# Performance work log

Measured on AMD Instinct MI355X. Metric: run time of the kernel, lower is better.

## Reference

```python
import jax, jax.numpy as jnp
import numpy as np

B, S, E = 2, 2048, 2048
H, D = 16, 128  # num_attention_heads, head_dim = hidden_size // num_heads


def rotate_half(x):
    x1 = x[..., : x.shape[-1] // 2]
    x2 = x[..., x.shape[-1] // 2 :]
    return jnp.concatenate((-x2, x1), axis=-1)


def setup_inputs() -> dict:
    key = jax.random.key(0)
    ks = jax.random.split(key, 7)
    return {
        "hidden_states": jax.random.normal(ks[0], (B, S, E), dtype=jnp.float32),
        "cos": jax.random.uniform(ks[1], (1, 1, S, D), dtype=jnp.float32),
        "sin": jax.random.uniform(ks[2], (1, 1, S, D), dtype=jnp.float32),
        "wq": jax.random.normal(ks[3], (E, H * D), dtype=jnp.float32) / np.sqrt(E),
        "wk": jax.random.normal(ks[4], (E, H * D), dtype=jnp.float32) / np.sqrt(E),
        "wv": jax.random.normal(ks[5], (E, H * D), dtype=jnp.float32) / np.sqrt(E),
        "wo": jax.random.normal(ks[6], (H * D, E), dtype=jnp.float32) / np.sqrt(H * D),
    }


def reference(hidden_states, cos, sin, wq, wk, wv, wo):
    # QKV projections (no bias, per attention_bias=False)
    q = (hidden_states @ wq).reshape(B, S, H, D).transpose(0, 2, 1, 3)  # bhsd
    k = (hidden_states @ wk).reshape(B, S, H, D).transpose(0, 2, 1, 3)
    v = (hidden_states @ wv).reshape(B, S, H, D).transpose(0, 2, 1, 3)
    # RoPE (applied after the head transpose, as in the original)
    q = q * cos + rotate_half(q) * sin
    k = k * cos + rotate_half(k) * sin
    # NOTE: original forward never applies self.scaling and uses no causal mask.
    scores = jnp.einsum("bhqd,bhkd->bhqk", q, k)
    attn = jax.nn.softmax(scores.astype(jnp.float32), axis=-1)
    out = jnp.einsum("bhqk,bhkd->bhqd", attn, v)
    out = out.transpose(0, 2, 1, 3).reshape(B, S, H * D)
    return out @ wo
```

## Files before the change

### kernel.cpp

```cpp
#include <hip/hip_runtime.h>
#include <stdint.h>

typedef _Float16 f16;
typedef _Float16 half8 __attribute__((ext_vector_type(8)));
typedef _Float16 half4 __attribute__((ext_vector_type(4)));
typedef __fp16 fp16x2 __attribute__((ext_vector_type(2)));
typedef float f32x4 __attribute__((ext_vector_type(4)));
typedef float f32x16 __attribute__((ext_vector_type(16)));
typedef uint32_t u32x4 __attribute__((ext_vector_type(4)));

static constexpr int Bsz = 2, S = 2048, E = 2048, H = 16, D = 128;
static constexpr int M = Bsz * S;
static constexpr int N_QKV = 3 * H * D;
static constexpr int HD = H * D;

__device__ __forceinline__ void gload_lds16(const void* gp, void* lp) {
  __builtin_amdgcn_global_load_lds(
      (const __attribute__((address_space(1))) uint32_t*)(uintptr_t)gp,
      (__attribute__((address_space(3))) uint32_t*)(uint32_t)(uintptr_t)lp,
      16, 0, 0);
}

__device__ __forceinline__ uint32_t pkrtz(float a, float b) {
  fp16x2 r = __builtin_amdgcn_cvt_pkrtz(a, b);
  return __builtin_bit_cast(uint32_t, r);
}

__global__ void cast_f32_f16(const float* __restrict__ in, f16* __restrict__ out) {
  size_t i = (size_t)(blockIdx.x * 256 + threadIdx.x) * 8;
  float4 a = *(const float4*)&in[i];
  float4 b = *(const float4*)&in[i + 4];
  half8 h;
  h[0] = (f16)a.x; h[1] = (f16)a.y; h[2] = (f16)a.z; h[3] = (f16)a.w;
  h[4] = (f16)b.x; h[5] = (f16)b.y; h[6] = (f16)b.z; h[7] = (f16)b.w;
  *(half8*)&out[i] = h;
}

__global__ void transpose_cast(const float* __restrict__ wq, const float* __restrict__ wk,
                               const float* __restrict__ wv, const float* __restrict__ wo,
                               f16* __restrict__ wt, f16* __restrict__ wot) {
  __shared__ float tile[32][33];
  int z = blockIdx.z;
  const float* src = (z == 0) ? wq : (z == 1) ? wk : (z == 2) ? wv : wo;
  f16* dst = (z == 3) ? wot : wt + (size_t)z * E * HD;
  int bx = blockIdx.x * 32, by = blockIdx.y * 32;
  int tx = threadIdx.x, ty = threadIdx.y;
#pragma unroll
  for (int r = 0; r < 4; ++r)
    tile[ty + r * 8][tx] = src[(size_t)(by + ty + r * 8) * 2048 + bx + tx];
  __syncthreads();
#pragma unroll
  for (int r = 0; r < 4; ++r)
    dst[(size_t)(bx + ty + r * 8) * 2048 + by + tx] = (f16)tile[tx][ty + r * 8];
}

template <typename OutT>
__global__ __launch_bounds__(256, 4) void gemm_bt(const f16* __restrict__ A,
                                                  const f16* __restrict__ Bt,
                                                  OutT* __restrict__ C,
                                                  int Mm, int Nn, int Kk) {
  __shared__ f16 As[128 * 32];
  __shared__ f16 Bs[128 * 32];
  const int t = threadIdx.x, l = t & 63;
  const int wm = (t >> 7) & 1, wn = (t >> 6) & 1;
  const int bm = blockIdx.x, bn = blockIdx.y;
  const int lr = l & 15, g = l >> 4;
  const int srow = t >> 2;
  const int schunk = t & 3;
  const int scol = ((schunk ^ (srow & 3)) * 8);
  const size_t abase = (size_t)(bm * 128 + srow) * Kk;
  const size_t bbase = (size_t)(bn * 128 + srow) * Kk;
  f32x4 acc[4][4] = {};
  for (int k0 = 0; k0 < Kk; k0 += 32) {
    __syncthreads();
    gload_lds16(&A[abase + k0 + scol], &As[t * 8]);
    gload_lds16(&A[abase + (size_t)64 * Kk + k0 + scol], &As[2048 + t * 8]);
    gload_lds16(&Bt[bbase + k0 + scol], &Bs[t * 8]);
    gload_lds16(&Bt[bbase + (size_t)64 * Kk + k0 + scol], &Bs[2048 + t * 8]);
    __syncthreads();
    half8 af[4], bf[4];
#pragma unroll
    for (int i = 0; i < 4; ++i) {
      int ra = wm * 64 + i * 16 + lr;
      int rb = wn * 64 + i * 16 + lr;
      af[i] = *(const half8*)&As[ra * 32 + ((g ^ (ra & 3)) * 8)];
      bf[i] = *(const half8*)&Bs[rb * 32 + ((g ^ (rb & 3)) * 8)];
    }
#pragma unroll
    for (int i = 0; i < 4; ++i)
#pragma unroll
      for (int j = 0; j < 4; ++j)
        acc[i][j] = __builtin_amdgcn_mfma_f32_16x16x32_f16(af[i], bf[j], acc[i][j], 0, 0, 0);
  }
#pragma unroll
  for (int i = 0; i < 4; ++i)
#pragma unroll
    for (int j = 0; j < 4; ++j) {
      int row = bm * 128 + wm * 64 + i * 16 + g * 4;
      int col = bn * 128 + wn * 64 + j * 16 + lr;
#pragma unroll
      for (int r = 0; r < 4; ++r)
        C[(size_t)(row + r) * Nn + col] = (OutT)acc[i][j][r];
    }
}

__global__ void rope_split(const f16* __restrict__ qkv, const float* __restrict__ cosb,
                           const float* __restrict__ sinb, f16* __restrict__ Q,
                           f16* __restrict__ Ko) {
  int idx = blockIdx.x * 256 + threadIdx.x;
  int d4 = idx & 15;
  int h = (idx >> 4) & 15;
  int s = (idx >> 8) & 2047;
  int b = idx >> 19;
  int d = d4 * 4;
  size_t mrow = (size_t)(b * S + s) * N_QKV;
  const f16* q = &qkv[mrow + h * D];
  const f16* k = &qkv[mrow + HD + h * D];
  size_t ob = ((size_t)(b * H + h) * S + s) * D;
  float4 c1 = *(const float4*)&cosb[s * D + d];
  float4 c2 = *(const float4*)&cosb[s * D + 64 + d];
  float4 s1 = *(const float4*)&sinb[s * D + d];
  float4 s2 = *(const float4*)&sinb[s * D + 64 + d];
  float c1a[4] = {c1.x, c1.y, c1.z, c1.w}, c2a[4] = {c2.x, c2.y, c2.z, c2.w};
  float s1a[4] = {s1.x, s1.y, s1.z, s1.w}, s2a[4] = {s2.x, s2.y, s2.z, s2.w};
  half4 qlo = *(const half4*)&q[d], qhi = *(const half4*)&q[d + 64];
  half4 klo = *(const half4*)&k[d], khi = *(const half4*)&k[d + 64];
  half4 oql, oqh, okl, okh;
#pragma unroll
  for (int j = 0; j < 4; ++j) {
    float ql = (float)qlo[j], qh = (float)qhi[j];
    float kl = (float)klo[j], kh = (float)khi[j];
    oql[j] = (f16)(ql * c1a[j] - qh * s1a[j]);
    oqh[j] = (f16)(qh * c2a[j] + ql * s2a[j]);
    okl[j] = (f16)(kl * c1a[j] - kh * s1a[j]);
    okh[j] = (f16)(kh * c2a[j] + kl * s2a[j]);
  }
  *(half4*)&Q[ob + d] = oql;  *(half4*)&Q[ob + d + 64] = oqh;
  *(half4*)&Ko[ob + d] = okl; *(half4*)&Ko[ob + d + 64] = okh;
}

__global__ void transpose_v(const f16* __restrict__ qkv, f16* __restrict__ VtG) {
  __shared__ f16 tl[64][136];
  int bid = blockIdx.x;
  int bh = bid >> 5, st = bid & 31;
  int b = bh >> 4, h = bh & 15;
  int t = threadIdx.x;
  int s0 = st * 64;
#pragma unroll
  for (int rnd = 0; rnd < 4; ++rnd) {
    int row = rnd * 16 + (t >> 4);
    int ch = t & 15;
    half8 v = *(const half8*)&qkv[(size_t)(b * S + s0 + row) * N_QKV + 2 * HD + h * D + ch * 8];
    *(half8*)&tl[row][ch * 8] = v;
  }
  __syncthreads();
#pragma unroll
  for (int rnd = 0; rnd < 4; ++rnd) {
    int d = rnd * 32 + (t >> 3);
    int ch = t & 7;
    half8 v;
#pragma unroll
    for (int j = 0; j < 8; ++j) v[j] = tl[ch * 8 + j][d];
    *(half8*)&VtG[((size_t)bh * D + d) * S + s0 + ch * 8] = v;
  }
}

__device__ __forceinline__ void stage_kv(const f16* __restrict__ Kg, const f16* __restrict__ Vg,
                                         f16* KsB, f16* VsB, int t, int kv) {
#pragma unroll
  for (int rnd = 0; rnd < 4; ++rnd) {
    int row = rnd * 16 + (t >> 4);
    int c = t & 15;
    gload_lds16(&Kg[(size_t)(kv + row) * D + ((c ^ (row & 7)) * 8)], &KsB[rnd * 2048 + t * 8]);
  }
#pragma unroll
  for (int rnd = 0; rnd < 4; ++rnd) {
    int row = rnd * 32 + (t >> 3);
    int c = t & 7;
    gload_lds16(&Vg[(size_t)row * S + kv + ((c ^ (row & 7)) * 8)], &VsB[rnd * 2048 + t * 8]);
  }
}

__global__ __launch_bounds__(256, 2) void flash_attn2(const f16* __restrict__ Q,
                                                      const f16* __restrict__ K,
                                                      const f16* __restrict__ Vt,
                                                      f16* __restrict__ O) {
  __shared__ f16 lds[2][16384];
  const int t = threadIdx.x, l = t & 63, w = t >> 6;
  const int c = l & 31, hi = l >> 5;
  int bid = blockIdx.x;
  bid = (bid & 7) * 64 + (bid >> 3);
  const int bh = bid >> 4, qt = bid & 15;
  const size_t baseQ = (size_t)bh * S * D;
  const f16* Kg = K + baseQ;
  const f16* Vg = Vt + (size_t)bh * D * S;
  const int q0 = qt * 128 + w * 32;
  half8 qf[8];
#pragma unroll
  for (int dc = 0; dc < 8; ++dc)
    qf[dc] = *(const half8*)&Q[baseQ + (size_t)(q0 + c) * D + dc * 16 + hi * 8];
  f32x16 o[4] = {};
  float m = -3.0e38f, ssum = 0.f;

  stage_kv(Kg, Vg, &lds[0][0], &lds[0][8192], t, 0);
  __syncthreads();

  for (int it = 0; it < S / 64; ++it) {
    const int cur = it & 1;
    const f16* KsB = &lds[cur][0];
    const f16* VsB = &lds[cur][8192];
    if (it + 1 < S / 64) stage_kv(Kg, Vg, &lds[cur ^ 1][0], &lds[cur ^ 1][8192], t, (it + 1) * 64);

    f32x16 s0 = {}, s1 = {};
    __builtin_amdgcn_s_setprio(1);
#pragma unroll
    for (int dc = 0; dc < 8; ++dc) {
      const int r0 = c, r1 = 32 + c;
      half8 kf0 = *(const half8*)&KsB[r0 * 128 + (((2 * dc + hi) ^ (r0 & 7)) * 8)];
      half8 kf1 = *(const half8*)&KsB[r1 * 128 + (((2 * dc + hi) ^ (r1 & 7)) * 8)];
      s0 = __builtin_amdgcn_mfma_f32_32x32x16_f16(kf0, qf[dc], s0, 0, 0, 0);
      s1 = __builtin_amdgcn_mfma_f32_32x32x16_f16(kf1, qf[dc], s1, 0, 0, 0);
    }
    __builtin_amdgcn_s_setprio(0);

    float tm = s0[0];
#pragma unroll
    for (int r = 1; r < 16; ++r) tm = fmaxf(tm, s0[r]);
#pragma unroll
    for (int r = 0; r < 16; ++r) tm = fmaxf(tm, s1[r]);
    tm = fmaxf(tm, __shfl_xor(tm, 32));
    float mn = fmaxf(m, tm);
    float corr = __expf(m - mn);
    m = mn;
    float ts = 0.f;
#pragma unroll
    for (int r = 0; r < 16; ++r) { s0[r] = __expf(s0[r] - mn); ts += s0[r]; }
#pragma unroll
    for (int r = 0; r < 16; ++r) { s1[r] = __expf(s1[r] - mn); ts += s1[r]; }
    ts += __shfl_xor(ts, 32);
    ssum = ssum * corr + ts;
#pragma unroll
    for (int dt = 0; dt < 4; ++dt)
#pragma unroll
      for (int r = 0; r < 16; ++r) o[dt][r] *= corr;

    half8 pf[4];
#pragma unroll
    for (int ks = 0; ks < 4; ++ks) {
      const int B0 = 2 * (ks & 1), B1 = B0 + 1;
      uint32_t X0, X1, Y0, Y1;
      if (ks < 2) {
        X0 = pkrtz(s0[4 * B0 + 0], s0[4 * B0 + 1]);
        X1 = pkrtz(s0[4 * B0 + 2], s0[4 * B0 + 3]);
        Y0 = pkrtz(s0[4 * B1 + 0], s0[4 * B1 + 1]);
        Y1 = pkrtz(s0[4 * B1 + 2], s0[4 * B1 + 3]);
      } else {
        X0 = pkrtz(s1[4 * B0 + 0], s1[4 * B0 + 1]);
        X1 = pkrtz(s1[4 * B0 + 2], s1[4 * B0 + 3]);
        Y0 = pkrtz(s1[4 * B1 + 0], s1[4 * B1 + 1]);
        Y1 = pkrtz(s1[4 * B1 + 2], s1[4 * B1 + 3]);
      }
      asm volatile("v_permlane32_swap_b32 %0, %1" : "+v"(X0), "+v"(Y0));
      asm volatile("v_permlane32_swap_b32 %0, %1" : "+v"(X1), "+v"(Y1));
      u32x4 pw; pw[0] = X0; pw[1] = X1; pw[2] = Y0; pw[3] = Y1;
      pf[ks] = __builtin_bit_cast(half8, pw);
    }

    __builtin_amdgcn_s_setprio(1);
#pragma unroll
    for (int dt = 0; dt < 4; ++dt) {
      const int row = dt * 32 + c;
#pragma unroll
      for (int ks = 0; ks < 4; ++ks) {
        half8 vf = *(const half8*)&VsB[row * 64 + (((2 * ks + hi) ^ (row & 7)) * 8)];
        o[dt] = __builtin_amdgcn_mfma_f32_32x32x16_f16(vf, pf[ks], o[dt], 0, 0, 0);
      }
    }
    __builtin_amdgcn_s_setprio(0);
    __syncthreads();
  }

  const float inv = 1.f / ssum;
  const int b = bh >> 4, h = bh & 15;
  const size_t orow = ((size_t)(b * S + q0 + c)) * HD + h * D;
#pragma unroll
  for (int dt = 0; dt < 4; ++dt)
#pragma unroll
    for (int b2 = 0; b2 < 4; ++b2) {
      half4 h4;
#pragma unroll
      for (int a = 0; a < 4; ++a) h4[a] = (f16)(o[dt][4 * b2 + a] * inv);
      *(half4*)&O[orow + dt * 32 + 8 * b2 + 4 * hi] = h4;
    }
}

extern "C" void kernel_launch(void* const* d_in, const int* in_sizes, int n_in,
                              void* d_out, int out_size, void* d_ws, size_t ws_size,
                              hipStream_t stream) {
  (void)in_sizes; (void)n_in; (void)out_size; (void)ws_size;
  const float* hs = (const float*)d_in[0];
  const float* cosb = (const float*)d_in[1];
  const float* sinb = (const float*)d_in[2];
  const float* wq = (const float*)d_in[3];
  const float* wk = (const float*)d_in[4];
  const float* wv = (const float*)d_in[5];
  const float* wo = (const float*)d_in[6];
  float* out = (float*)d_out;
  char* ws = (char*)d_ws;
  f16* hs16 = (f16*)(ws);
  f16* attn = (f16*)(ws);
  f16* wt   = (f16*)(ws + (16u << 20));
  f16* wot  = (f16*)(ws + (40u << 20));
  f16* qkv  = (f16*)(ws + (48u << 20));
  f16* Qb   = (f16*)(ws + (96u << 20));
  f16* Kb   = (f16*)(ws + (112u << 20));
  f16* VtG  = (f16*)(ws + (128u << 20));

  cast_f32_f16<<<dim3(4096), dim3(256), 0, stream>>>(hs, hs16);
  transpose_cast<<<dim3(64, 64, 4), dim3(32, 8), 0, stream>>>(wq, wk, wv, wo, wt, wot);
  gemm_bt<f16><<<dim3(32, 48), dim3(256), 0, stream>>>(hs16, wt, qkv, M, N_QKV, E);
  rope_split<<<dim3(4096), dim3(256), 0, stream>>>(qkv, cosb, sinb, Qb, Kb);
  transpose_v<<<dim3(1024), dim3(256), 0, stream>>>(qkv, VtG);
  flash_attn2<<<dim3(512), dim3(256), 0, stream>>>(Qb, Kb, VtG, attn);
  gemm_bt<float><<<dim3(32, 16), dim3(256), 0, stream>>>(attn, wot, out, M, E, HD);
}
```

Before: 308.8 us.

## Add pipelined 256x192 QKV GEMM, widen output GEMM K-step, lazy softmax rescale

Replaces the QKV projection GEMM with a new 512-thread kernel using 256x192 tiles. It double-buffers LDS, issues global-to-LDS loads ahead of the MFMA phases with explicit vmcnt waits, and remaps block IDs so neighbouring blocks share tiles. The output-projection GEMM now stages 64 K-elements per barrier pair and uses a swizzled block order for cache locality. In flash attention, the running max and the O/sum rescale update only when a new tile's max exceeds the old one by more than a threshold. This skips exp and multiply work, but unnormalized exponentials can reach up to e^8.

```diff
diff --git a/kernel.cpp b/kernel.cpp
--- a/kernel.cpp
+++ b/kernel.cpp
@@ -54,54 +54,112 @@
     dst[(size_t)(bx + ty + r * 8) * 2048 + by + tx] = (f16)tile[tx][ty + r * 8];
 }
 
-template <typename OutT>
-__global__ __launch_bounds__(256, 4) void gemm_bt(const f16* __restrict__ A,
-                                                  const f16* __restrict__ Bt,
-                                                  OutT* __restrict__ C,
-                                                  int Mm, int Nn, int Kk) {
-  __shared__ f16 As[128 * 32];
-  __shared__ f16 Bs[128 * 32];
-  const int t = threadIdx.x, l = t & 63;
-  const int wm = (t >> 7) & 1, wn = (t >> 6) & 1;
-  const int bm = blockIdx.x, bn = blockIdx.y;
+__global__ __launch_bounds__(512, 1) void gemm8(const f16* __restrict__ A,
+                                                const f16* __restrict__ Bt,
+                                                f16* __restrict__ C) {
+  __shared__ f16 lds[57344];
+  const int Kk = 2048;
+  const int NT = 32;
+  const int t = threadIdx.x, l = t & 63, wv = t >> 6;
+  const int wm = wv >> 2, wn = wv & 3;
   const int lr = l & 15, g = l >> 4;
-  const int srow = t >> 2;
-  const int schunk = t & 3;
-  const int scol = ((schunk ^ (srow & 3)) * 8);
-  const size_t abase = (size_t)(bm * 128 + srow) * Kk;
-  const size_t bbase = (size_t)(bn * 128 + srow) * Kk;
-  f32x4 acc[4][4] = {};
-  for (int k0 = 0; k0 < Kk; k0 += 32) {
-    __syncthreads();
-    gload_lds16(&A[abase + k0 + scol], &As[t * 8]);
-    gload_lds16(&A[abase + (size_t)64 * Kk + k0 + scol], &As[2048 + t * 8]);
-    gload_lds16(&Bt[bbase + k0 + scol], &Bs[t * 8]);
-    gload_lds16(&Bt[bbase + (size_t)64 * Kk + k0 + scol], &Bs[2048 + t * 8]);
-    __syncthreads();
-    half8 af[4], bf[4];
-#pragma unroll
-    for (int i = 0; i < 4; ++i) {
-      int ra = wm * 64 + i * 16 + lr;
-      int rb = wn * 64 + i * 16 + lr;
-      af[i] = *(const half8*)&As[ra * 32 + ((g ^ (ra & 3)) * 8)];
-      bf[i] = *(const half8*)&Bs[rb * 32 + ((g ^ (rb & 3)) * 8)];
-    }
-#pragma unroll
-    for (int i = 0; i < 4; ++i)
-#pragma unroll
-      for (int j = 0; j < 4; ++j)
-        acc[i][j] = __builtin_amdgcn_mfma_f32_16x16x32_f16(af[i], bf[j], acc[i][j], 0, 0, 0);
-  }
-#pragma unroll
-  for (int i = 0; i < 4; ++i)
-#pragma unroll
-    for (int j = 0; j < 4; ++j) {
-      int row = bm * 128 + wm * 64 + i * 16 + g * 4;
-      int col = bn * 128 + wn * 64 + j * 16 + lr;
+  const int bid = blockIdx.x;
+  const int ii = bid >> 3;
+  const int bm = (bid & 7) * 2 + (ii & 1);
+  const int bn = ii >> 1;
+  const int arow = t >> 1, ah = t & 1;
+  const int fa = (arow >> 2) & 3;
+  const int ca0 = (ah ^ fa) * 8;
+  const int ca1 = ((2 | ah) ^ fa) * 8;
+  const f16* Abase = A + (size_t)(bm * 256 + arow) * Kk;
+  const int brl = t >> 3, bc = t & 7;
+  const int cbx = (bc ^ (brl & 7)) * 8;
+  const f16* Bs0 = Bt + (size_t)(bn * 192 + brl) * Kk + cbx;
+  const f16* Bs1 = Bt + (size_t)(bn * 192 + 64 + brl) * Kk + cbx;
+  const f16* Bs2 = Bt + (size_t)(bn * 192 + 128 + brl) * Kk + cbx;
+
+#define ABUF(b_, kh_) ((b_) * 16384 + (kh_) * 8192)
+#define BBUF(b_) (32768 + (b_) * 12288)
+#define STAGE_A(T_, kh_)                                                     \
+  do {                                                                       \
+    int ko_ = (T_) * 64 + (kh_) * 32;                                        \
+    int bb_ = (T_) & 1;                                                      \
+    gload_lds16(Abase + ko_ + ca0, &lds[ABUF(bb_, kh_) + t * 8]);            \
+    gload_lds16(Abase + ko_ + ca1, &lds[ABUF(bb_, kh_) + 4096 + t * 8]);     \
+  } while (0)
+#define STAGE_B(T_)                                                          \
+  do {                                                                       \
+    int ko_ = (T_) * 64;                                                     \
+    int bb_ = (T_) & 1;                                                      \
+    gload_lds16(Bs0 + ko_, &lds[BBUF(bb_) + t * 8]);                         \
+    gload_lds16(Bs1 + ko_, &lds[BBUF(bb_) + 4096 + t * 8]);                  \
+    gload_lds16(Bs2 + ko_, &lds[BBUF(bb_) + 8192 + t * 8]);                  \
+  } while (0)
+#define LDA(mq_, kh_)                                                        \
+  _Pragma("unroll") for (int i2 = 0; i2 < 4; ++i2) {                         \
+    int ra = wm * 128 + ((mq_)*4 + i2) * 16 + lr;                            \
+    int s_ = g ^ ((ra >> 2) & 3);                                            \
+    af[i2] = *(const half8*)&lds[ABUF(cb, kh_) + (s_ >> 1) * 4096 + ra * 16 + (s_ & 1) * 8]; \
+  }
+#define LDB(kh_)                                                             \
+  _Pragma("unroll") for (int nj = 0; nj < 3; ++nj) {                         \
+    int rb = wn * 48 + nj * 16 + lr;                                         \
+    bf[nj] = *(const half8*)&lds[BBUF(cb) + rb * 64 + (((kh_)*4 + g) ^ (rb & 7)) * 8]; \
+  }
+#define MM(mq_)                                                              \
+  __builtin_amdgcn_s_setprio(1);                                             \
+  _Pragma("unroll") for (int i2 = 0; i2 < 4; ++i2)                           \
+  _Pragma("unroll") for (int nj = 0; nj < 3; ++nj)                           \
+      acc[(mq_)*4 + i2][nj] =                                                \
+          __builtin_amdgcn_mfma_f32_16x16x32_f16(af[i2], bf[nj], acc[(mq_)*4 + i2][nj], 0, 0, 0); \
+  __builtin_amdgcn_s_setprio(0);
+#define BAR() __builtin_amdgcn_s_barrier()
+#define VM7() asm volatile("s_waitcnt vmcnt(7)" ::: "memory")
+#define VM0() asm volatile("s_waitcnt vmcnt(0)" ::: "memory")
+
+  f32x4 acc[8][3] = {};
+  STAGE_A(0, 0); STAGE_A(0, 1); STAGE_B(0);
+  STAGE_A(1, 0); STAGE_B(1);
+  asm volatile("s_waitcnt vmcnt(5)" ::: "memory");
+  BAR();
+
+  for (int T = 0; T < NT; ++T) {
+    const int cb = T & 1;
+    half8 af[4], bf[3];
+    LDA(0, 0); LDB(0);
+    if (T + 1 < NT) STAGE_A(T + 1, 1);
+    BAR(); MM(0); BAR();
+    LDA(1, 0);
+    if (T >= NT - 3) { VM0(); } else { VM7(); }
+    BAR(); MM(1); BAR();
+    LDA(0, 1); LDB(1);
+    if (T + 2 < NT) STAGE_A(T + 2, 0);
+    BAR(); MM(0); BAR();
+    LDA(1, 1);
+    if (T + 2 < NT) STAGE_B(T + 2);
+    if (T >= NT - 3) { VM0(); } else { VM7(); }
+    BAR(); MM(1); BAR();
+  }
+
+  const int crow = bm * 256 + wm * 128 + g * 4;
+  const int ccol = bn * 192 + wn * 48 + lr;
+#pragma unroll
+  for (int mi = 0; mi < 8; ++mi)
+#pragma unroll
+    for (int nj = 0; nj < 3; ++nj)
 #pragma unroll
       for (int r = 0; r < 4; ++r)
-        C[(size_t)(row + r) * Nn + col] = (OutT)acc[i][j][r];
-    }
+        C[(size_t)(crow + mi * 16 + r) * N_QKV + ccol + nj * 16] = (f16)acc[mi][nj][r];
+#undef ABUF
+#undef BBUF
+#undef STAGE_A
+#undef STAGE_B
+#undef LDA
+#undef LDB
+#undef MM
+#undef BAR
+#undef VM7
+#undef VM0
 }
 
 __global__ void rope_split(const f16* __restrict__ qkv, const float* __restrict__ cosb,
@@ -165,6 +223,65 @@
   }
 }
 
+#define STAGE4(PTR, BASE, KOFF, DST)                                       \
+  gload_lds16(&PTR[BASE + (KOFF) + scol], &DST[t * 8]);                    \
+  gload_lds16(&PTR[BASE + (size_t)64 * Kk + (KOFF) + scol], &DST[2048 + t * 8]);
+
+template <typename OutT>
+__global__ __launch_bounds__(256, 4) void gemm_bt(const f16* __restrict__ A,
+                                                  const f16* __restrict__ Bt,
+                                                  OutT* __restrict__ C,
+                                                  int Nn, int Kk) {
+  __shared__ f16 As[8192];
+  __shared__ f16 Bs[8192];
+  const int t = threadIdx.x, l = t & 63;
+  const int wm = (t >> 7) & 1, wn = (t >> 6) & 1;
+  const int bid = blockIdx.x;
+  const int bm = (bid & 7) * 4 + ((bid >> 3) & 3);
+  const int bn = bid >> 5;
+  const int lr = l & 15, g = l >> 4;
+  const int srow = t >> 2;
+  const int scol = (((t & 3) ^ (srow & 3)) * 8);
+  const size_t abase = (size_t)(bm * 128 + srow) * Kk;
+  const size_t bbase = (size_t)(bn * 128 + srow) * Kk;
+  f32x4 acc[4][4] = {};
+  for (int k0 = 0; k0 < Kk; k0 += 64) {
+    __syncthreads();
+    STAGE4(A, abase, k0, As);
+    STAGE4(Bt, bbase, k0, Bs);
+    STAGE4(A, abase, k0 + 32, (As + 4096));
+    STAGE4(Bt, bbase, k0 + 32, (Bs + 4096));
+    __syncthreads();
+#pragma unroll
+    for (int kh = 0; kh < 2; ++kh) {
+      const int so = kh * 4096;
+      half8 af[4], bf[4];
+#pragma unroll
+      for (int i = 0; i < 4; ++i) {
+        int ra = wm * 64 + i * 16 + lr;
+        int rb = wn * 64 + i * 16 + lr;
+        af[i] = *(const half8*)&As[so + ra * 32 + ((g ^ (ra & 3)) * 8)];
+        bf[i] = *(const half8*)&Bs[so + rb * 32 + ((g ^ (rb & 3)) * 8)];
+      }
+#pragma unroll
+      for (int i = 0; i < 4; ++i)
+#pragma unroll
+        for (int j = 0; j < 4; ++j)
+          acc[i][j] = __builtin_amdgcn_mfma_f32_16x16x32_f16(af[i], bf[j], acc[i][j], 0, 0, 0);
+    }
+  }
+#pragma unroll
+  for (int i = 0; i < 4; ++i)
+#pragma unroll
+    for (int j = 0; j < 4; ++j) {
+      int row = bm * 128 + wm * 64 + i * 16 + g * 4;
+      int col = bn * 128 + wn * 64 + j * 16 + lr;
+#pragma unroll
+      for (int r = 0; r < 4; ++r)
+        C[(size_t)(row + r) * Nn + col] = (OutT)acc[i][j][r];
+    }
+}
+
 __device__ __forceinline__ void stage_kv(const f16* __restrict__ Kg, const f16* __restrict__ Vg,
                                          f16* KsB, f16* VsB, int t, int kv) {
 #pragma unroll
@@ -229,20 +346,23 @@
 #pragma unroll
     for (int r = 0; r < 16; ++r) tm = fmaxf(tm, s1[r]);
     tm = fmaxf(tm, __shfl_xor(tm, 32));
-    float mn = fmaxf(m, tm);
-    float corr = __expf(m - mn);
-    m = mn;
+    if (!__all(tm <= m + 8.f)) {
+      float mn = fmaxf(m, tm);
+      float corr = __expf(m - mn);
+      m = mn;
+      ssum *= corr;
+#pragma unroll
+      for (int dt = 0; dt < 4; ++dt)
+#pragma unroll
+        for (int r = 0; r < 16; ++r) o[dt][r] *= corr;
+    }
     float ts = 0.f;
 #pragma unroll
-    for (int r = 0; r < 16; ++r) { s0[r] = __expf(s0[r] - mn); ts += s0[r]; }
-#pragma unroll
-    for (int r = 0; r < 16; ++r) { s1[r] = __expf(s1[r] - mn); ts += s1[r]; }
+    for (int r = 0; r < 16; ++r) { s0[r] = __expf(s0[r] - m); ts += s0[r]; }
+#pragma unroll
+    for (int r = 0; r < 16; ++r) { s1[r] = __expf(s1[r] - m); ts += s1[r]; }
     ts += __shfl_xor(ts, 32);
-    ssum = ssum * corr + ts;
-#pragma unroll
-    for (int dt = 0; dt < 4; ++dt)
-#pragma unroll
-      for (int r = 0; r < 16; ++r) o[dt][r] *= corr;
+    ssum += ts;
 
     half8 pf[4];
 #pragma unroll
@@ -318,9 +438,9 @@
 
   cast_f32_f16<<<dim3(4096), dim3(256), 0, stream>>>(hs, hs16);
   transpose_cast<<<dim3(64, 64, 4), dim3(32, 8), 0, stream>>>(wq, wk, wv, wo, wt, wot);
-  gemm_bt<f16><<<dim3(32, 48), dim3(256), 0, stream>>>(hs16, wt, qkv, M, N_QKV, E);
+  gemm8<<<dim3(512), dim3(512), 0, stream>>>(hs16, wt, qkv);
   rope_split<<<dim3(4096), dim3(256), 0, stream>>>(qkv, cosb, sinb, Qb, Kb);
   transpose_v<<<dim3(1024), dim3(256), 0, stream>>>(qkv, VtG);
   flash_attn2<<<dim3(512), dim3(256), 0, stream>>>(Qb, Kb, VtG, attn);
-  gemm_bt<float><<<dim3(32, 16), dim3(256), 0, stream>>>(attn, wot, out, M, E, HD);
-}
+  gemm_bt<float><<<dim3(512), dim3(256), 0, stream>>>(attn, wot, out, E, HD);
+}
```

Result: faster. 282.0 us (-8.7%).
